# Kernel tuning notes

Hardware: AMD Instinct MI355X
Metric: run time of the kernel (lower is better)

## Reference

```python
import jax, jax.numpy as jnp
import numpy as np

EPS = 1e-5

def _conv_bn_relu(x, w, gamma, beta):
    # x: [B, C, N], w: [O, C] (1x1 conv, no bias)
    y = jnp.einsum('oc,bcn->bon', w, x)
    # BatchNorm1d in training mode: per-channel stats over (B, N)
    mean = jnp.mean(y, axis=(0, 2), keepdims=True)
    var = jnp.var(y, axis=(0, 2), keepdims=True)
    yhat = (y - mean) * jax.lax.rsqrt(var + EPS)
    return jax.nn.relu(gamma[None, :, None] * yhat + beta[None, :, None])


def setup_inputs() -> dict:
    key = jax.random.key(0)
    ks = jax.random.split(key, 8)
    B, C, N, Cr = 4, 256, 4096, 32
    x = jax.random.normal(ks[0], (B, C, N), dtype=jnp.float32)
    w1 = jax.random.normal(ks[1], (Cr, C), dtype=jnp.float32) * (1.0 / np.sqrt(C))
    w2 = jax.random.normal(ks[2], (Cr, C), dtype=jnp.float32) * (1.0 / np.sqrt(C))
    w3 = jax.random.normal(ks[3], (C, C), dtype=jnp.float32) * (1.0 / np.sqrt(C))
    g1 = 1.0 + 0.1 * jax.random.normal(ks[4], (Cr,), dtype=jnp.float32)
    b1 = 0.1 * jax.random.normal(ks[5], (Cr,), dtype=jnp.float32)
    g2 = 1.0 + 0.1 * jax.random.normal(ks[6], (Cr,), dtype=jnp.float32)
    b2 = 0.1 * jax.random.normal(ks[7], (Cr,), dtype=jnp.float32)
    g3 = jnp.ones((C,), dtype=jnp.float32)
    b3 = jnp.zeros((C,), dtype=jnp.float32)
    return {'x': x, 'w1': w1, 'w2': w2, 'w3': w3,
            'g1': g1, 'b1': b1, 'g2': g2, 'b2': b2, 'g3': g3, 'b3': b3}


def reference(x, w1, w2, w3, g1, b1, g2, b2, g3, b3):
    # a: [B, N, Cr] (queries), k: [B, Cr, N] (keys)
    a = _conv_bn_relu(x, w1, g1, b1).transpose(0, 2, 1)
    k = _conv_bn_relu(x, w2, g2, b2)
    # s[b, n, m] = softmax_m(sum_c a[b,n,c] * k[b,c,m])
    s = jax.nn.softmax(jnp.einsum('bnc,bcm->bnm', a, k), axis=-1)
    d = _conv_bn_relu(x, w3, g3, b3)  # [B, C, N]
    # out = x + d @ s^T : out[b,c,m] = sum_n d[b,c,n] * s[m,n]
    out = x + jnp.einsum('bcn,bmn->bcm', d, s)
    return out
```

## Files before the change

### kernel.cpp

```cpp
#include <hip/hip_runtime.h>
#include <cstddef>
#include <cstdint>

#define B_ 4
#define C_ 256
#define N_ 4096
#define KF_OFF_B  ((size_t)1024 * 1024)
#define DF_OFF_B  ((size_t)2 * 1024 * 1024)
#define SUM_OFF_B ((size_t)10 * 1024 * 1024)
#define ML_OFF_B  (SUM_OFF_B + 1280 * 4)
#define XH_OFF_B  (ML_OFF_B + 524288)
#define XL_OFF_B  (XH_OFF_B + (size_t)8 * 1024 * 1024)
#define WH_OFF_B  (XL_OFF_B + (size_t)8 * 1024 * 1024)
#define WL_OFF_B  (WH_OFF_B + 163840)
#define LOG2E 1.4426950408889634f

typedef unsigned short bfraw;
typedef __attribute__((ext_vector_type(8))) short short8;
typedef __attribute__((ext_vector_type(4))) float float4v;
typedef __attribute__((ext_vector_type(4))) bfraw bfraw4;

__device__ inline bfraw f2bf(float f) {
    union { float f; uint32_t u; } c; c.f = f;
    uint32_t u = c.u;
    u += 0x7fffu + ((u >> 16) & 1u);
    return (bfraw)(u >> 16);
}
__device__ inline float bf2f(bfraw h) {
    union { uint32_t u; float f; } c; c.u = ((uint32_t)h) << 16;
    return c.f;
}
#if __has_builtin(__builtin_amdgcn_exp2f)
__device__ inline float EXP2(float x) { return __builtin_amdgcn_exp2f(x); }
#else
__device__ inline float EXP2(float x) { return exp2f(x); }
#endif
__device__ inline uint32_t pack2(float a, float b) {
    union { float f; uint32_t u; } ca, cb; ca.f = a; cb.f = b;
#if __has_builtin(__builtin_amdgcn_perm)
    return __builtin_amdgcn_perm(cb.u + 0x8000u, ca.u + 0x8000u, 0x07060302u);
#else
    return ((ca.u + 0x8000u) >> 16) | ((cb.u + 0x8000u) & 0xffff0000u);
#endif
}

__global__ __launch_bounds__(256) void wsplit_kernel(
    const float* __restrict__ w1, const float* __restrict__ w2,
    const float* __restrict__ w3, uint8_t* __restrict__ wsb)
{
    bfraw* wh = (bfraw*)(wsb + WH_OFF_B);
    bfraw* wl = (bfraw*)(wsb + WL_OFF_B);
    if (blockIdx.x == 0) {
        float* sums = (float*)(wsb + SUM_OFF_B);
        for (int i = threadIdx.x; i < 640; i += 256) sums[i] = 0.f;
    }
    int idx4 = (blockIdx.x * 256 + threadIdx.x) * 4;
    int ch = idx4 >> 8, k = idx4 & 255;
    const float* wr = (ch < 32) ? (w1 + ch * C_)
                      : (ch < 64) ? (w2 + (ch - 32) * C_)
                                  : (w3 + (ch - 64) * C_);
    float4 v = *(const float4*)&wr[k];
    float va[4] = {v.x, v.y, v.z, v.w};
    bfraw4 h, l;
#pragma unroll
    for (int j = 0; j < 4; ++j) {
        h[j] = f2bf(va[j]);
        l[j] = f2bf(va[j] - bf2f(h[j]));
    }
    *(bfraw4*)&wh[idx4] = h;
    *(bfraw4*)&wl[idx4] = l;
}

__global__ __launch_bounds__(256) void xtsplit_kernel(
    const float* __restrict__ x, uint8_t* __restrict__ wsb)
{
    __shared__ float Ls[64][65];
    bfraw* xh = (bfraw*)(wsb + XH_OFF_B);
    bfraw* xl = (bfraw*)(wsb + XL_OFF_B);
    const int id = blockIdx.x;
    const int b  = id >> 8;
    const int c0 = ((id >> 6) & 3) << 6;
    const int n0 = (id & 63) << 6;
    const int t  = threadIdx.x;
    {
        int cl = t >> 4, nc = (t & 15) << 2;
#pragma unroll
        for (int i = 0; i < 4; ++i) {
            float4 v = *(const float4*)&x[((size_t)b * C_ + c0 + cl + i * 16) * N_ + n0 + nc];
            Ls[cl + i * 16][nc + 0] = v.x;
            Ls[cl + i * 16][nc + 1] = v.y;
            Ls[cl + i * 16][nc + 2] = v.z;
            Ls[cl + i * 16][nc + 3] = v.w;
        }
    }
    __syncthreads();
    int nl = t >> 2, seg = t & 3;
    bfraw hb[16], lb[16];
#pragma unroll
    for (int j = 0; j < 16; ++j) {
        float v = Ls[seg * 16 + j][nl];
        bfraw h = f2bf(v);
        hb[j] = h;
        lb[j] = f2bf(v - bf2f(h));
    }
    size_t base = ((size_t)b * N_ + n0 + nl) * 256 + c0 + seg * 16;
    *(short8*)&xh[base]     = *(short8*)&hb[0];
    *(short8*)&xh[base + 8] = *(short8*)&hb[8];
    *(short8*)&xl[base]     = *(short8*)&lb[0];
    *(short8*)&xl[base + 8] = *(short8*)&lb[8];
}

__global__ __launch_bounds__(256, 2) void ygemm_kernel(uint8_t* __restrict__ wsb)
{
    const bfraw* xh = (const bfraw*)(wsb + XH_OFF_B);
    const bfraw* xl = (const bfraw*)(wsb + XL_OFF_B);
    const bfraw* wh = (const bfraw*)(wsb + WH_OFF_B);
    const bfraw* wl = (const bfraw*)(wsb + WL_OFF_B);
    bfraw* qf  = (bfraw*)wsb;
    bfraw* kfp = (bfraw*)(wsb + KF_OFF_B);
    bfraw* dfp = (bfraw*)(wsb + DF_OFF_B);
    float* sums  = (float*)(wsb + SUM_OFF_B);
    float* sumsq = sums + 320;
    __shared__ float redS[4][64], redQ[4][64];

    const int bx = blockIdx.x;
    const int by = blockIdx.y;
    const int b  = bx >> 5;
    const int n0 = (bx << 7) & (N_ - 1);
    const int t = threadIdx.x, w = t >> 6, l = t & 63, lq = l & 15, lg = l >> 4;
    const int nw = n0 + w * 32;

    float4v acc[4][2];
#pragma unroll
    for (int i = 0; i < 4; ++i)
#pragma unroll
        for (int j = 0; j < 2; ++j) acc[i][j] = (float4v){0.f, 0.f, 0.f, 0.f};

    for (int s = 0; s < 8; ++s) {
        const int k0 = s * 32;
        short8 ah[4], al[4], bh[2], bl[2];
#pragma unroll
        for (int ct = 0; ct < 4; ++ct) {
            size_t off = (size_t)(by * 64 + ct * 16 + lq) * 256 + k0 + lg * 8;
            ah[ct] = *(const short8*)&wh[off];
            al[ct] = *(const short8*)&wl[off];
        }
#pragma unroll
        for (int nt = 0; nt < 2; ++nt) {
            size_t off = ((size_t)b * N_ + nw + nt * 16 + lq) * 256 + k0 + lg * 8;
            bh[nt] = *(const short8*)&xh[off];
            bl[nt] = *(const short8*)&xl[off];
        }
#pragma unroll
        for (int ct = 0; ct < 4; ++ct)
#pragma unroll
            for (int nt = 0; nt < 2; ++nt) {
                acc[ct][nt] = __builtin_amdgcn_mfma_f32_16x16x32_bf16(ah[ct], bh[nt], acc[ct][nt], 0, 0, 0);
                acc[ct][nt] = __builtin_amdgcn_mfma_f32_16x16x32_bf16(al[ct], bh[nt], acc[ct][nt], 0, 0, 0);
                acc[ct][nt] = __builtin_amdgcn_mfma_f32_16x16x32_bf16(ah[ct], bl[nt], acc[ct][nt], 0, 0, 0);
            }
    }
#pragma unroll
    for (int ct = 0; ct < 4; ++ct) {
        float sv[4], qv[4];
#pragma unroll
        for (int r = 0; r < 4; ++r) {
            float a0 = acc[ct][0][r], a1 = acc[ct][1][r];
            sv[r] = a0 + a1;
            qv[r] = a0 * a0 + a1 * a1;
#pragma unroll
            for (int m = 1; m < 16; m <<= 1) {
                sv[r] += __shfl_xor(sv[r], m);
                qv[r] += __shfl_xor(qv[r], m);
            }
        }
        if (lq == 0) {
#pragma unroll
            for (int r = 0; r < 4; ++r) {
                redS[w][ct * 16 + lg * 4 + r] = sv[r];
                redQ[w][ct * 16 + lg * 4 + r] = qv[r];
            }
        }
    }
    __syncthreads();
    if (t < 64) {
        float s = redS[0][t] + redS[1][t] + redS[2][t] + redS[3][t];
        float q = redQ[0][t] + redQ[1][t] + redQ[2][t] + redQ[3][t];
        atomicAdd(&sums[by * 64 + t], s);
        atomicAdd(&sumsq[by * 64 + t], q);
    }
    if (by == 0) {
#pragma unroll
        for (int ct = 0; ct < 4; ++ct)
#pragma unroll
            for (int nt = 0; nt < 2; ++nt)
#pragma unroll
                for (int r = 0; r < 4; ++r) {
                    int c = ct * 16 + lg * 4 + r;
                    int n = nw + nt * 16 + lq;
                    size_t addr = ((size_t)(b << 8) + (n >> 4)) * 512
                                + (size_t)(((n & 15) | (((c >> 3) & 3) << 4)) << 3) + (c & 7);
                    bfraw v = f2bf(acc[ct][nt][r]);
                    if (c < 32) qf[addr] = v; else kfp[addr] = v;
                }
    } else {
#pragma unroll
        for (int ct = 0; ct < 4; ++ct)
#pragma unroll
            for (int nt = 0; nt < 2; ++nt)
#pragma unroll
                for (int r = 0; r < 4; ++r) {
                    int cg = (by - 1) * 64 + ct * 16 + lg * 4 + r;
                    int n = nw + nt * 16 + lq;
                    size_t addr = (((size_t)(b << 4) + (cg >> 4)) * 128 + (n >> 5)) * 512
                                + (size_t)(((cg & 15) | (((n >> 3) & 3) << 4)) << 3) + (n & 7);
                    dfp[addr] = f2bf(acc[ct][nt][r]);
                }
    }
}

__device__ inline void bn_coef(const float* __restrict__ sums,
                               const float* __restrict__ g1, const float* __restrict__ b1,
                               const float* __restrict__ g2, const float* __restrict__ b2,
                               const float* __restrict__ g3, const float* __restrict__ b3,
                               int ch, float& sc, float& bi)
{
    const float inv = 1.0f / (float)(B_ * N_);
    float mean = sums[ch] * inv;
    float var  = sums[320 + ch] * inv - mean * mean;
    float g, bb;
    if (ch < 32)      { g = g1[ch];      bb = b1[ch]; }
    else if (ch < 64) { g = g2[ch - 32]; bb = b2[ch - 32]; }
    else              { g = g3[ch - 64]; bb = b3[ch - 64]; }
    sc = g * rsqrtf(var + 1e-5f);
    bi = bb - sc * mean;
    if (ch < 32) { sc *= LOG2E; bi *= LOG2E; }
}

__global__ __launch_bounds__(256) void affine_kernel(
    uint8_t* __restrict__ wsb,
    const float* __restrict__ g1, const float* __restrict__ b1,
    const float* __restrict__ g2, const float* __restrict__ b2,
    const float* __restrict__ g3, const float* __restrict__ b3)
{
    bfraw* base = (bfraw*)wsb;
    const float* sums = (const float*)(wsb + SUM_OFF_B);
    size_t i8 = ((size_t)blockIdx.x * 256 + threadIdx.x) * 8;
    bfraw4 v0 = *(bfraw4*)&base[i8];
    bfraw4 v1 = *(bfraw4*)&base[i8 + 4];
    if (i8 < 1048576) {
        int ch0 = (((int)(i8 >> 7)) & 3) * 8 + ((i8 < 524288) ? 0 : 32);
        float sa[8], ca[8];
#pragma unroll
        for (int j = 0; j < 8; ++j)
            bn_coef(sums, g1, b1, g2, b2, g3, b3, ch0 + j, sa[j], ca[j]);
#pragma unroll
        for (int j = 0; j < 4; ++j) {
            v0[j] = f2bf(fmaxf(0.f, fmaf(sa[j],     bf2f(v0[j]), ca[j])));
            v1[j] = f2bf(fmaxf(0.f, fmaf(sa[j + 4], bf2f(v1[j]), ca[j + 4])));
        }
    } else {
        size_t rel = i8 - 1048576;
        int ch = 64 + (((int)(rel >> 16)) & 15) * 16 + (((int)(rel >> 3)) & 15);
        float s, b;
        bn_coef(sums, g1, b1, g2, b2, g3, b3, ch, s, b);
#pragma unroll
        for (int j = 0; j < 4; ++j) {
            v0[j] = f2bf(fmaxf(0.f, fmaf(s, bf2f(v0[j]), b)));
            v1[j] = f2bf(fmaxf(0.f, fmaf(s, bf2f(v1[j]), b)));
        }
    }
    *(bfraw4*)&base[i8] = v0;
    *(bfraw4*)&base[i8 + 4] = v1;
}

__global__ __launch_bounds__(256, 4) void mlpass_kernel(uint8_t* __restrict__ wsb)
{
    const bfraw* qf  = (const bfraw*)wsb;
    const bfraw* kfp = (const bfraw*)(wsb + KF_OFF_B);
    float* mpart = (float*)(wsb + ML_OFF_B);
    float* lpart = mpart + 65536;
    const int id = blockIdx.x;
    const int b = id & 3;
    const int ks = (id >> 2) & 3;
    const int n0q = (id >> 4) << 6;
    const int tid = threadIdx.x;
    const int w = tid >> 6, l = tid & 63, lq = l & 15, lg = l >> 4;
    const short8 qfrag = *(const short8*)&qf[((size_t)(b * 256 + (n0q >> 4) + w)) * 512 + l * 8];

    float mx = -1e30f, sum = 0.f;
    const int tbeg = b * 256 + ks * 64;
    for (int tk = tbeg; tk < tbeg + 64; tk += 8) {
        float4v st[8];
#pragma unroll
        for (int kt = 0; kt < 8; ++kt) {
            short8 kf = *(const short8*)&kfp[((size_t)(tk + kt)) * 512 + l * 8];
            float4v z = {0.f, 0.f, 0.f, 0.f};
            st[kt] = __builtin_amdgcn_mfma_f32_16x16x32_bf16(kf, qfrag, z, 0, 0, 0);
        }
        float m1 = st[0][0];
#pragma unroll
        for (int kt = 0; kt < 8; ++kt)
#pragma unroll
            for (int r = 0; r < 4; ++r) m1 = fmaxf(m1, st[kt][r]);
        float nm = fmaxf(mx, m1);
        float ae = 0.f;
#pragma unroll
        for (int kt = 0; kt < 8; ++kt)
#pragma unroll
            for (int r = 0; r < 4; ++r) ae += EXP2(st[kt][r] - nm);
        sum = sum * EXP2(mx - nm) + ae;
        mx = nm;
    }
#pragma unroll
    for (int m = 16; m < 64; m <<= 1) {
        float mo = __shfl_xor(mx, m);
        float so = __shfl_xor(sum, m);
        float nm = fmaxf(mx, mo);
        sum = sum * EXP2(mx - nm) + so * EXP2(mo - nm);
        mx = nm;
    }
    if (lg == 0) {
        int idx = ks * 16384 + b * N_ + n0q + w * 16 + lq;
        mpart[idx] = mx;
        lpart[idx] = sum;
    }
}

__global__ __launch_bounds__(512) void flash_kernel(
    const float* __restrict__ x, const uint8_t* __restrict__ wsb,
    float* __restrict__ out)
{
    const bfraw* qf  = (const bfraw*)wsb;
    const bfraw* kfp = (const bfraw*)(wsb + KF_OFF_B);
    const bfraw* dfp = (const bfraw*)(wsb + DF_OFF_B);
    const float* mpart = (const float*)(wsb + ML_OFF_B);
    const float* lpart = mpart + 65536;
    __shared__ bfraw Pl[2][64 * 128];

    const int id  = blockIdx.x;
    const int b   = id & 3;
    const int n0q = (id >> 2) << 6;
    const int tid = threadIdx.x;
    const int w   = tid >> 6;
    const int l   = tid & 63;
    const int lq  = l & 15;
    const int lg  = l >> 4;
    const int sw  = lq & 7;
    const int qt_s    = w >> 1;
    const int ks_loc  = w & 1;
    const int ctg0 = w;
    const int ctg1 = 8 + w;

    const short8 qfrag = *(const short8*)&qf[((size_t)(b * 256 + (n0q >> 4) + qt_s)) * 512 + l * 8];

    float mlq;
    {
        int qi = b * N_ + n0q + qt_s * 16 + lq;
        float M = -1e30f, ms[4], ls[4];
#pragma unroll
        for (int s = 0; s < 4; ++s) {
            ms[s] = mpart[s * 16384 + qi];
            ls[s] = lpart[s * 16384 + qi];
            M = fmaxf(M, ms[s]);
        }
        float L = 0.f;
#pragma unroll
        for (int s = 0; s < 4; ++s) L += ls[s] * EXP2(ms[s] - M);
        mlq = M + __log2f(L);
    }
    const float4v zv = {-mlq, -mlq, -mlq, -mlq};

    float4v acc[2][4];
#pragma unroll
    for (int i = 0; i < 2; ++i)
#pragma unroll
        for (int j = 0; j < 4; ++j) acc[i][j] = (float4v){0.f, 0.f, 0.f, 0.f};

    short8 kfr[4], dfr[2][4];
#pragma unroll
    for (int kt = 0; kt < 4; ++kt)
        kfr[kt] = *(const short8*)&kfp[((size_t)(b * 256 + ks_loc * 4 + kt)) * 512 + l * 8];
#pragma unroll
    for (int ch = 0; ch < 4; ++ch) {
        dfr[0][ch] = *(const short8*)&dfp[(((size_t)(b * 16 + ctg0)) * 128 + ch) * 512 + l * 8];
        dfr[1][ch] = *(const short8*)&dfp[(((size_t)(b * 16 + ctg1)) * 128 + ch) * 512 + l * 8];
    }

    const int qrow = qt_s * 16 + lq;
    for (int it = 0; it < 32; ++it) {
        const int ib = it & 1;
        const int nit = (it + 1) & 31;
        float4v st[4];
#pragma unroll
        for (int kt = 0; kt < 4; ++kt)
            st[kt] = __builtin_amdgcn_mfma_f32_16x16x32_bf16(kfr[kt], qfrag, zv, 0, 0, 0);
#pragma unroll
        for (int kt = 0; kt < 4; ++kt)
            kfr[kt] = *(const short8*)&kfp[((size_t)(b * 256 + nit * 8 + ks_loc * 4 + kt)) * 512 + l * 8];
#pragma unroll
        for (int kt = 0; kt < 4; ++kt) {
            float e0 = EXP2(st[kt][0]);
            float e1 = EXP2(st[kt][1]);
            float e2 = EXP2(st[kt][2]);
            float e3 = EXP2(st[kt][3]);
            uint2 pd = {pack2(e0, e1), pack2(e2, e3)};
            int g = (2 * (ks_loc * 4 + kt) + (lg >> 1)) ^ sw;
            *(uint2*)&Pl[ib][qrow * 128 + g * 8 + (lg & 1) * 4] = pd;
        }
        __syncthreads();
#pragma unroll
        for (int ch = 0; ch < 4; ++ch) {
            short8 bfr[4];
            int g = (ch * 4 + lg) ^ sw;
#pragma unroll
            for (int qt = 0; qt < 4; ++qt)
                bfr[qt] = *(const short8*)&Pl[ib][(qt * 16 + lq) * 128 + g * 8];
            __builtin_amdgcn_s_setprio(1);
#pragma unroll
            for (int qt = 0; qt < 4; ++qt) {
                acc[0][qt] = __builtin_amdgcn_mfma_f32_16x16x32_bf16(dfr[0][ch], bfr[qt], acc[0][qt], 0, 0, 0);
                acc[1][qt] = __builtin_amdgcn_mfma_f32_16x16x32_bf16(dfr[1][ch], bfr[qt], acc[1][qt], 0, 0, 0);
            }
            __builtin_amdgcn_s_setprio(0);
            dfr[0][ch] = *(const short8*)&dfp[(((size_t)(b * 16 + ctg0)) * 128 + nit * 4 + ch) * 512 + l * 8];
            dfr[1][ch] = *(const short8*)&dfp[(((size_t)(b * 16 + ctg1)) * 128 + nit * 4 + ch) * 512 + l * 8];
        }
    }
#pragma unroll
    for (int ct = 0; ct < 2; ++ct) {
        int ctg = ct ? ctg1 : ctg0;
#pragma unroll
        for (int r = 0; r < 4; ++r) {
            int c = ctg * 16 + lg * 4 + r;
            size_t base = ((size_t)b * C_ + c) * N_ + n0q;
#pragma unroll
            for (int qt = 0; qt < 4; ++qt) {
                size_t idx = base + qt * 16 + lq;
                out[idx] = x[idx] + acc[ct][qt][r];
            }
        }
    }
}

extern "C" void kernel_launch(void* const* d_in, const int* in_sizes, int n_in,
                              void* d_out, int out_size, void* d_ws, size_t ws_size,
                              hipStream_t stream) {
    (void)in_sizes; (void)n_in; (void)out_size; (void)ws_size;
    const float* x  = (const float*)d_in[0];
    const float* w1 = (const float*)d_in[1];
    const float* w2 = (const float*)d_in[2];
    const float* w3 = (const float*)d_in[3];
    const float* g1 = (const float*)d_in[4];
    const float* b1 = (const float*)d_in[5];
    const float* g2 = (const float*)d_in[6];
    const float* b2 = (const float*)d_in[7];
    const float* g3 = (const float*)d_in[8];
    const float* b3 = (const float*)d_in[9];
    uint8_t* wsb = (uint8_t*)d_ws;
    float* outp = (float*)d_out;

    wsplit_kernel<<<80, 256, 0, stream>>>(w1, w2, w3, wsb);
    xtsplit_kernel<<<1024, 256, 0, stream>>>(x, wsb);
    ygemm_kernel<<<dim3(128, 5), 256, 0, stream>>>(wsb);
    affine_kernel<<<2560, 256, 0, stream>>>(wsb, g1, b1, g2, b2, g3, b3);
    mlpass_kernel<<<1024, 256, 0, stream>>>(wsb);
    flash_kernel<<<256, 512, 0, stream>>>(x, wsb, outp);
}
```

Before: 184.3 us.

## Replace separate max/sum pass with online softmax inside flash kernel

Removes the mlpass kernel that precomputed per-query softmax max and normalizer. The flash kernel now tracks a running max with lazy rescaling, triggered only when scores exceed a threshold, and a running sum per key-split half. The two halves are combined at the end and the accumulators normalized. It also stages K tiles through shared memory with double buffering and merges the weight-split and x-split prep kernels into one launch. Launch count and the second pass over K drop, at the cost of extra registers (two accumulator sets), extra shared memory and occasional rescale work.

```diff
diff --git a/kernel.cpp b/kernel.cpp
--- a/kernel.cpp
+++ b/kernel.cpp
@@ -44,37 +44,37 @@
 #endif
 }
 
-__global__ __launch_bounds__(256) void wsplit_kernel(
+__global__ __launch_bounds__(256) void prep_kernel(
+    const float* __restrict__ x,
     const float* __restrict__ w1, const float* __restrict__ w2,
     const float* __restrict__ w3, uint8_t* __restrict__ wsb)
 {
-    bfraw* wh = (bfraw*)(wsb + WH_OFF_B);
-    bfraw* wl = (bfraw*)(wsb + WL_OFF_B);
-    if (blockIdx.x == 0) {
-        float* sums = (float*)(wsb + SUM_OFF_B);
-        for (int i = threadIdx.x; i < 640; i += 256) sums[i] = 0.f;
-    }
-    int idx4 = (blockIdx.x * 256 + threadIdx.x) * 4;
-    int ch = idx4 >> 8, k = idx4 & 255;
-    const float* wr = (ch < 32) ? (w1 + ch * C_)
-                      : (ch < 64) ? (w2 + (ch - 32) * C_)
-                                  : (w3 + (ch - 64) * C_);
-    float4 v = *(const float4*)&wr[k];
-    float va[4] = {v.x, v.y, v.z, v.w};
-    bfraw4 h, l;
-#pragma unroll
-    for (int j = 0; j < 4; ++j) {
-        h[j] = f2bf(va[j]);
-        l[j] = f2bf(va[j] - bf2f(h[j]));
-    }
-    *(bfraw4*)&wh[idx4] = h;
-    *(bfraw4*)&wl[idx4] = l;
-}
-
-__global__ __launch_bounds__(256) void xtsplit_kernel(
-    const float* __restrict__ x, uint8_t* __restrict__ wsb)
-{
     __shared__ float Ls[64][65];
+    if (blockIdx.x >= 1024) {
+        int bid = blockIdx.x - 1024;
+        if (bid == 0) {
+            float* sums = (float*)(wsb + SUM_OFF_B);
+            for (int i = threadIdx.x; i < 640; i += 256) sums[i] = 0.f;
+        }
+        bfraw* wh = (bfraw*)(wsb + WH_OFF_B);
+        bfraw* wl = (bfraw*)(wsb + WL_OFF_B);
+        int idx4 = (bid * 256 + threadIdx.x) * 4;
+        int ch = idx4 >> 8, k = idx4 & 255;
+        const float* wr = (ch < 32) ? (w1 + ch * C_)
+                          : (ch < 64) ? (w2 + (ch - 32) * C_)
+                                      : (w3 + (ch - 64) * C_);
+        float4 v = *(const float4*)&wr[k];
+        float va[4] = {v.x, v.y, v.z, v.w};
+        bfraw4 h, l;
+#pragma unroll
+        for (int j = 0; j < 4; ++j) {
+            h[j] = f2bf(va[j]);
+            l[j] = f2bf(va[j] - bf2f(h[j]));
+        }
+        *(bfraw4*)&wh[idx4] = h;
+        *(bfraw4*)&wl[idx4] = l;
+        return;
+    }
     bfraw* xh = (bfraw*)(wsb + XH_OFF_B);
     bfraw* xl = (bfraw*)(wsb + XL_OFF_B);
     const int id = blockIdx.x;
@@ -274,69 +274,18 @@
     *(bfraw4*)&base[i8 + 4] = v1;
 }
 
-__global__ __launch_bounds__(256, 4) void mlpass_kernel(uint8_t* __restrict__ wsb)
-{
-    const bfraw* qf  = (const bfraw*)wsb;
-    const bfraw* kfp = (const bfraw*)(wsb + KF_OFF_B);
-    float* mpart = (float*)(wsb + ML_OFF_B);
-    float* lpart = mpart + 65536;
-    const int id = blockIdx.x;
-    const int b = id & 3;
-    const int ks = (id >> 2) & 3;
-    const int n0q = (id >> 4) << 6;
-    const int tid = threadIdx.x;
-    const int w = tid >> 6, l = tid & 63, lq = l & 15, lg = l >> 4;
-    const short8 qfrag = *(const short8*)&qf[((size_t)(b * 256 + (n0q >> 4) + w)) * 512 + l * 8];
-
-    float mx = -1e30f, sum = 0.f;
-    const int tbeg = b * 256 + ks * 64;
-    for (int tk = tbeg; tk < tbeg + 64; tk += 8) {
-        float4v st[8];
-#pragma unroll
-        for (int kt = 0; kt < 8; ++kt) {
-            short8 kf = *(const short8*)&kfp[((size_t)(tk + kt)) * 512 + l * 8];
-            float4v z = {0.f, 0.f, 0.f, 0.f};
-            st[kt] = __builtin_amdgcn_mfma_f32_16x16x32_bf16(kf, qfrag, z, 0, 0, 0);
-        }
-        float m1 = st[0][0];
-#pragma unroll
-        for (int kt = 0; kt < 8; ++kt)
-#pragma unroll
-            for (int r = 0; r < 4; ++r) m1 = fmaxf(m1, st[kt][r]);
-        float nm = fmaxf(mx, m1);
-        float ae = 0.f;
-#pragma unroll
-        for (int kt = 0; kt < 8; ++kt)
-#pragma unroll
-            for (int r = 0; r < 4; ++r) ae += EXP2(st[kt][r] - nm);
-        sum = sum * EXP2(mx - nm) + ae;
-        mx = nm;
-    }
-#pragma unroll
-    for (int m = 16; m < 64; m <<= 1) {
-        float mo = __shfl_xor(mx, m);
-        float so = __shfl_xor(sum, m);
-        float nm = fmaxf(mx, mo);
-        sum = sum * EXP2(mx - nm) + so * EXP2(mo - nm);
-        mx = nm;
-    }
-    if (lg == 0) {
-        int idx = ks * 16384 + b * N_ + n0q + w * 16 + lq;
-        mpart[idx] = mx;
-        lpart[idx] = sum;
-    }
-}
-
-__global__ __launch_bounds__(512) void flash_kernel(
+__global__ __launch_bounds__(512, 2) void flash_kernel(
     const float* __restrict__ x, const uint8_t* __restrict__ wsb,
     float* __restrict__ out)
 {
     const bfraw* qf  = (const bfraw*)wsb;
     const bfraw* kfp = (const bfraw*)(wsb + KF_OFF_B);
     const bfraw* dfp = (const bfraw*)(wsb + DF_OFF_B);
-    const float* mpart = (const float*)(wsb + ML_OFF_B);
-    const float* lpart = mpart + 65536;
     __shared__ bfraw Pl[2][64 * 128];
+    __shared__ bfraw kst[2][8 * 512];
+    __shared__ float mfac[2][2][64];
+    __shared__ uint2 flagw[2];
+    __shared__ float msh[2][64], lsh[2][64];
 
     const int id  = blockIdx.x;
     const int b   = id & 3;
@@ -347,68 +296,104 @@
     const int lq  = l & 15;
     const int lg  = l >> 4;
     const int sw  = lq & 7;
-    const int qt_s    = w >> 1;
-    const int ks_loc  = w & 1;
+    const int qt_s   = w >> 1;
+    const int ks_loc = w & 1;
     const int ctg0 = w;
     const int ctg1 = 8 + w;
 
     const short8 qfrag = *(const short8*)&qf[((size_t)(b * 256 + (n0q >> 4) + qt_s)) * 512 + l * 8];
 
-    float mlq;
-    {
-        int qi = b * N_ + n0q + qt_s * 16 + lq;
-        float M = -1e30f, ms[4], ls[4];
-#pragma unroll
-        for (int s = 0; s < 4; ++s) {
-            ms[s] = mpart[s * 16384 + qi];
-            ls[s] = lpart[s * 16384 + qi];
-            M = fmaxf(M, ms[s]);
-        }
-        float L = 0.f;
-#pragma unroll
-        for (int s = 0; s < 4; ++s) L += ls[s] * EXP2(ms[s] - M);
-        mlq = M + __log2f(L);
-    }
-    const float4v zv = {-mlq, -mlq, -mlq, -mlq};
-
-    float4v acc[2][4];
+    float m = 0.f, ps = 0.f;
+    float4v zv = {0.f, 0.f, 0.f, 0.f};
+
+    float4v accA[2][4], accB[2][4];
 #pragma unroll
     for (int i = 0; i < 2; ++i)
 #pragma unroll
-        for (int j = 0; j < 4; ++j) acc[i][j] = (float4v){0.f, 0.f, 0.f, 0.f};
-
-    short8 kfr[4], dfr[2][4];
-#pragma unroll
-    for (int kt = 0; kt < 4; ++kt)
-        kfr[kt] = *(const short8*)&kfp[((size_t)(b * 256 + ks_loc * 4 + kt)) * 512 + l * 8];
+        for (int j = 0; j < 4; ++j) {
+            accA[i][j] = (float4v){0.f, 0.f, 0.f, 0.f};
+            accB[i][j] = (float4v){0.f, 0.f, 0.f, 0.f};
+        }
+
+    short8 dfr[2][4];
 #pragma unroll
     for (int ch = 0; ch < 4; ++ch) {
         dfr[0][ch] = *(const short8*)&dfp[(((size_t)(b * 16 + ctg0)) * 128 + ch) * 512 + l * 8];
         dfr[1][ch] = *(const short8*)&dfp[(((size_t)(b * 16 + ctg1)) * 128 + ch) * 512 + l * 8];
     }
+    {
+        short8 v = *(const short8*)&kfp[((size_t)(b * 256 + w)) * 512 + l * 8];
+        *(short8*)&kst[0][w * 512 + l * 8] = v;
+    }
+    __syncthreads();
 
     const int qrow = qt_s * 16 + lq;
     for (int it = 0; it < 32; ++it) {
         const int ib = it & 1;
         const int nit = (it + 1) & 31;
+        short8 kstage = *(const short8*)&kfp[((size_t)(b * 256 + nit * 8 + w)) * 512 + l * 8];
+        short8 kfr[4];
+#pragma unroll
+        for (int kt = 0; kt < 4; ++kt)
+            kfr[kt] = *(const short8*)&kst[ib][(ks_loc * 4 + kt) * 512 + l * 8];
         float4v st[4];
 #pragma unroll
         for (int kt = 0; kt < 4; ++kt)
             st[kt] = __builtin_amdgcn_mfma_f32_16x16x32_bf16(kfr[kt], qfrag, zv, 0, 0, 0);
+        float pm = st[0][0];
 #pragma unroll
         for (int kt = 0; kt < 4; ++kt)
-            kfr[kt] = *(const short8*)&kfp[((size_t)(b * 256 + nit * 8 + ks_loc * 4 + kt)) * 512 + l * 8];
+#pragma unroll
+            for (int r = 0; r < 4; ++r) pm = fmaxf(pm, st[kt][r]);
+        pm = fmaxf(pm, __shfl_xor(pm, 16));
+        pm = fmaxf(pm, __shfl_xor(pm, 32));
+        const int resc = __any(pm > 8.0f);
+        float f = 1.0f;
+        if (resc) {
+            float d = fmaxf(pm, 0.f);
+            f = EXP2(-d);
+            ps *= f;
+#pragma unroll
+            for (int kt = 0; kt < 4; ++kt)
+#pragma unroll
+                for (int r = 0; r < 4; ++r) st[kt][r] -= d;
+            m += d;
+#pragma unroll
+            for (int r = 0; r < 4; ++r) zv[r] -= d;
+        }
 #pragma unroll
         for (int kt = 0; kt < 4; ++kt) {
             float e0 = EXP2(st[kt][0]);
             float e1 = EXP2(st[kt][1]);
             float e2 = EXP2(st[kt][2]);
             float e3 = EXP2(st[kt][3]);
+            ps += (e0 + e1) + (e2 + e3);
             uint2 pd = {pack2(e0, e1), pack2(e2, e3)};
             int g = (2 * (ks_loc * 4 + kt) + (lg >> 1)) ^ sw;
             *(uint2*)&Pl[ib][qrow * 128 + g * 8 + (lg & 1) * 4] = pd;
         }
+        if (lg == 0) mfac[ib][ks_loc][qrow] = f;
+        if (l == 0) ((unsigned char*)&flagw[ib])[ks_loc * 4 + qt_s] = (unsigned char)resc;
+        *(short8*)&kst[ib ^ 1][w * 512 + l * 8] = kstage;
         __syncthreads();
+        uint2 fw = flagw[ib];
+        if (fw.x | fw.y) {
+            float fA[4], fB[4];
+#pragma unroll
+            for (int j = 0; j < 4; ++j) {
+                fA[j] = mfac[ib][0][j * 16 + lq];
+                fB[j] = mfac[ib][1][j * 16 + lq];
+            }
+#pragma unroll
+            for (int ct = 0; ct < 2; ++ct)
+#pragma unroll
+                for (int j = 0; j < 4; ++j)
+#pragma unroll
+                    for (int r = 0; r < 4; ++r) {
+                        accA[ct][j][r] *= fA[j];
+                        accB[ct][j][r] *= fB[j];
+                    }
+        }
 #pragma unroll
         for (int ch = 0; ch < 4; ++ch) {
             short8 bfr[4];
@@ -417,16 +402,39 @@
             for (int qt = 0; qt < 4; ++qt)
                 bfr[qt] = *(const short8*)&Pl[ib][(qt * 16 + lq) * 128 + g * 8];
             __builtin_amdgcn_s_setprio(1);
-#pragma unroll
-            for (int qt = 0; qt < 4; ++qt) {
-                acc[0][qt] = __builtin_amdgcn_mfma_f32_16x16x32_bf16(dfr[0][ch], bfr[qt], acc[0][qt], 0, 0, 0);
-                acc[1][qt] = __builtin_amdgcn_mfma_f32_16x16x32_bf16(dfr[1][ch], bfr[qt], acc[1][qt], 0, 0, 0);
+            if (ch < 2) {
+#pragma unroll
+                for (int qt = 0; qt < 4; ++qt) {
+                    accA[0][qt] = __builtin_amdgcn_mfma_f32_16x16x32_bf16(dfr[0][ch], bfr[qt], accA[0][qt], 0, 0, 0);
+                    accA[1][qt] = __builtin_amdgcn_mfma_f32_16x16x32_bf16(dfr[1][ch], bfr[qt], accA[1][qt], 0, 0, 0);
+                }
+            } else {
+#pragma unroll
+                for (int qt = 0; qt < 4; ++qt) {
+                    accB[0][qt] = __builtin_amdgcn_mfma_f32_16x16x32_bf16(dfr[0][ch], bfr[qt], accB[0][qt], 0, 0, 0);
+                    accB[1][qt] = __builtin_amdgcn_mfma_f32_16x16x32_bf16(dfr[1][ch], bfr[qt], accB[1][qt], 0, 0, 0);
+                }
             }
             __builtin_amdgcn_s_setprio(0);
             dfr[0][ch] = *(const short8*)&dfp[(((size_t)(b * 16 + ctg0)) * 128 + nit * 4 + ch) * 512 + l * 8];
             dfr[1][ch] = *(const short8*)&dfp[(((size_t)(b * 16 + ctg1)) * 128 + nit * 4 + ch) * 512 + l * 8];
         }
     }
+    ps += __shfl_xor(ps, 16);
+    ps += __shfl_xor(ps, 32);
+    if (lg == 0) { msh[ks_loc][qrow] = m; lsh[ks_loc][qrow] = ps; }
+    __syncthreads();
+    float rA[4], rB[4];
+#pragma unroll
+    for (int qt = 0; qt < 4; ++qt) {
+        float m0 = msh[0][qt * 16 + lq], m1 = msh[1][qt * 16 + lq];
+        float l0 = lsh[0][qt * 16 + lq], l1 = lsh[1][qt * 16 + lq];
+        float M = fmaxf(m0, m1);
+        float sA = EXP2(m0 - M), sB = EXP2(m1 - M);
+        float inv = 1.0f / (l0 * sA + l1 * sB);
+        rA[qt] = sA * inv;
+        rB[qt] = sB * inv;
+    }
 #pragma unroll
     for (int ct = 0; ct < 2; ++ct) {
         int ctg = ct ? ctg1 : ctg0;
@@ -437,7 +445,7 @@
 #pragma unroll
             for (int qt = 0; qt < 4; ++qt) {
                 size_t idx = base + qt * 16 + lq;
-                out[idx] = x[idx] + acc[ct][qt][r];
+                out[idx] = x[idx] + accA[ct][qt][r] * rA[qt] + accB[ct][qt][r] * rB[qt];
             }
         }
     }
@@ -460,10 +468,8 @@
     uint8_t* wsb = (uint8_t*)d_ws;
     float* outp = (float*)d_out;
 
-    wsplit_kernel<<<80, 256, 0, stream>>>(w1, w2, w3, wsb);
-    xtsplit_kernel<<<1024, 256, 0, stream>>>(x, wsb);
+    prep_kernel<<<1104, 256, 0, stream>>>(x, w1, w2, w3, wsb);
     ygemm_kernel<<<dim3(128, 5), 256, 0, stream>>>(wsb);
     affine_kernel<<<2560, 256, 0, stream>>>(wsb, g1, b1, g2, b2, g3, b3);
-    mlpass_kernel<<<1024, 256, 0, stream>>>(wsb);
     flash_kernel<<<256, 512, 0, stream>>>(x, wsb, outp);
 }
```

Measured after the change: 184.5 us. About the same (+0.1%).
